# Optimization experiments

Hardware: AMD Instinct MI355X
Metric: run time of the kernel (lower is better)

The kernel has to match this reference:

```python
import jax, jax.numpy as jnp
import numpy as np

N = 20000
E = 320000
IN_DIM = 512
HID = 64
HEADS = 8
OUT_DIM = 40
NEG_SLOPE = 0.2


def glorot(key, shape):
    fan = shape[0] + shape[-1] if len(shape) > 1 else shape[-1]
    s = jnp.sqrt(6.0 / fan)
    return jax.random.uniform(key, shape, jnp.float32, -s, s)


def setup_inputs() -> dict:
    key = jax.random.key(0)
    ks = jax.random.split(key, 12)
    x = jax.random.normal(ks[0], (N, IN_DIM), jnp.float32)
    edge_index = jax.random.randint(ks[1], (2, E), 0, N, jnp.int64)
    return {
        "x": x,
        "edge_index": edge_index,
        "W1": glorot(ks[2], (IN_DIM, HEADS * HID)),
        "att1_src": glorot(ks[3], (HEADS, HID)),
        "att1_dst": glorot(ks[4], (HEADS, HID)),
        "b1": jnp.zeros((HEADS * HID,), jnp.float32),
        "W2": glorot(ks[5], (HEADS * HID, HEADS * HID)),
        "att2_src": glorot(ks[6], (HEADS, HID)),
        "att2_dst": glorot(ks[7], (HEADS, HID)),
        "b2": jnp.zeros((HEADS * HID,), jnp.float32),
        "W3": glorot(ks[8], (HEADS * HID, OUT_DIM)),
        "att3_src": glorot(ks[9], (1, OUT_DIM)),
        "att3_dst": glorot(ks[10], (1, OUT_DIM)),
        "b3": jnp.zeros((OUT_DIM,), jnp.float32),
    }


def gat_conv(x, src, dst, W, att_src, att_dst, bias, heads, out_c):
    # h: [N, H, C] transformed node features
    h = (x @ W).reshape(N, heads, out_c)
    a_src = jnp.sum(h * att_src, axis=-1)  # [N, H]
    a_dst = jnp.sum(h * att_dst, axis=-1)  # [N, H]
    # edge logits (message j=src -> i=dst), softmax grouped by dst
    logits = jax.nn.leaky_relu(a_src[src] + a_dst[dst], NEG_SLOPE)  # [Etot, H]
    seg_max = jax.ops.segment_max(logits, dst, num_segments=N)
    seg_max = jnp.where(jnp.isfinite(seg_max), seg_max, 0.0)
    ex = jnp.exp(logits - seg_max[dst])
    denom = jax.ops.segment_sum(ex, dst, num_segments=N)
    alpha = ex / (denom[dst] + 1e-16)  # [Etot, H]
    msg = h[src] * alpha[:, :, None]  # [Etot, H, C]
    out = jax.ops.segment_sum(msg, dst, num_segments=N)  # [N, H, C]
    return out.reshape(N, heads * out_c) + bias


def reference(x, edge_index, W1, att1_src, att1_dst, b1,
              W2, att2_src, att2_dst, b2,
              W3, att3_src, att3_dst, b3):
    # add self loops (PyG GATConv default)
    loops = jnp.arange(N, dtype=edge_index.dtype)
    src = jnp.concatenate([edge_index[0], loops])
    dst = jnp.concatenate([edge_index[1], loops])
    # dropout layers are identity in eval mode
    h = jax.nn.elu(gat_conv(x, src, dst, W1, att1_src, att1_dst, b1, HEADS, HID))
    h = jax.nn.elu(gat_conv(h, src, dst, W2, att2_src, att2_dst, b2, HEADS, HID))
    h = gat_conv(h, src, dst, W3, att3_src, att3_dst, b3, 1, OUT_DIM)
    return jax.nn.log_softmax(h, axis=-1)
```

## Files before the change

kernel.cpp:

```cpp
#include <hip/hip_runtime.h>
#include <math.h>

#define NN 20000
#define EE 320000
#define ETOT (EE + NN)
#define NEG 0.2f

typedef unsigned short ushortT;
typedef __attribute__((ext_vector_type(8))) short short8v;
typedef __attribute__((ext_vector_type(8))) unsigned short u16x8;
typedef __attribute__((ext_vector_type(4))) float f32x4;

__device__ __forceinline__ ushortT f2b(float f){
  unsigned u = __float_as_uint(f);
  u += 0x7FFFu + ((u >> 16) & 1u);
  return (ushortT)(u >> 16);
}
__device__ __forceinline__ float b2f(ushortT b){
  return __uint_as_float(((unsigned)b) << 16);
}

__global__ void k_cvt(const float* __restrict__ in, ushortT* __restrict__ outp, int n4){
  int i = blockIdx.x*blockDim.x + threadIdx.x;
  if(i < n4){
    float4 v = *reinterpret_cast<const float4*>(in + (size_t)i*4);
    ushort4 o;
    o.x = f2b(v.x); o.y = f2b(v.y); o.z = f2b(v.z); o.w = f2b(v.w);
    *reinterpret_cast<ushort4*>(outp + (size_t)i*4) = o;
  }
}

__global__ void k_wtrans(const float* __restrict__ W, ushortT* __restrict__ Wt){
  __shared__ float t[32][33];
  int bk = blockIdx.x*32, bn = blockIdx.y*32;
  int tx = threadIdx.x & 31, ty = threadIdx.x >> 5;
  for(int r=0;r<32;r+=8)
    t[ty+r][tx] = W[(size_t)(bk+ty+r)*512 + bn+tx];
  __syncthreads();
  for(int r=0;r<32;r+=8)
    Wt[(size_t)(bn+ty+r)*512 + bk+tx] = f2b(t[tx][ty+r]);
}

__global__ void k_wtrans3(const float* __restrict__ W3, ushortT* __restrict__ Wt3p){
  int idx = blockIdx.x*blockDim.x + threadIdx.x;
  if(idx >= 64*48*8) return;
  int kslot = idx / 384;
  int rem = idx - kslot*384;
  int n = rem >> 3;
  int jj = rem & 7;
  int k = kslot*8 + jj;
  float v = (n < 40) ? W3[(size_t)k*40 + n] : 0.f;
  Wt3p[idx] = f2b(v);
}

__global__ void k_count(const int* __restrict__ edst, int* __restrict__ counts){
  int e = blockIdx.x*blockDim.x + threadIdx.x;
  if(e < ETOT){
    int d = (e < EE) ? edst[e] : (e - EE);
    atomicAdd(&counts[d], 1);
  }
}

__global__ void k_scan(const int* __restrict__ counts, int* __restrict__ rowstart){
  __shared__ int lds[1024];
  int tid = threadIdx.x;
  int base = tid*20;
  int s = 0;
  for(int j=0;j<20;j++){ int i=base+j; if(i<NN) s += counts[i]; }
  lds[tid] = s; __syncthreads();
  for(int off=1; off<1024; off<<=1){
    int v = (tid>=off) ? lds[tid-off] : 0;
    __syncthreads();
    lds[tid] += v;
    __syncthreads();
  }
  int run = lds[tid] - s;
  for(int j=0;j<20;j++){
    int i = base+j;
    if(i <= NN){
      rowstart[i] = run;
      if(i < NN) run += counts[i];
    }
  }
}

__global__ void k_fill(const int* __restrict__ esrc, const int* __restrict__ edst,
                       const int* __restrict__ rowstart,
                       int* __restrict__ cursor, int* __restrict__ srcs){
  int e = blockIdx.x*blockDim.x + threadIdx.x;
  if(e < ETOT){
    int d = (e < EE) ? edst[e] : (e - EE);
    int s = (e < EE) ? esrc[e] : (e - EE);
    int pos = rowstart[d] + atomicAdd(&cursor[d], 1);
    srcs[pos] = s;
  }
}

__global__ __launch_bounds__(256) void k_gemm_bf16(
    const ushortT* __restrict__ A, const ushortT* __restrict__ Bt,
    ushortT* __restrict__ Cb, int M)
{
  const int K = 512;
  __shared__ __align__(16) ushortT As[128*32];
  __shared__ __align__(16) ushortT Bs[128*32];
  int bm = blockIdx.x*128, bn = blockIdx.y*128;
  int tid = threadIdx.x, wave = tid>>6, lane = tid&63;
  int wm = (wave>>1)*64, wn = (wave&1)*64;
  f32x4 acc[4][4] = {};

  int l4 = lane>>2;
  int s4 = lane&3;
  int src_slot = s4 ^ (l4 & 3);
  int r16 = lane&15, kg = lane>>4;

  for(int k0=0;k0<K;k0+=32){
    #pragma unroll
    for(int c=0;c<2;c++){
      int chunk = wave*2 + c;
      int arow = bm + chunk*16 + l4; if(arow > M-1) arow = M-1;
      const ushortT* ga = A + (size_t)arow*K + k0 + src_slot*8;
      __builtin_amdgcn_global_load_lds(
          (const __attribute__((address_space(1))) void*)ga,
          (__attribute__((address_space(3))) void*)(As + chunk*16*32), 16, 0, 0);
      int brow = bn + chunk*16 + l4;
      const ushortT* gb = Bt + (size_t)brow*K + k0 + src_slot*8;
      __builtin_amdgcn_global_load_lds(
          (const __attribute__((address_space(1))) void*)gb,
          (__attribute__((address_space(3))) void*)(Bs + chunk*16*32), 16, 0, 0);
    }
    asm volatile("s_waitcnt vmcnt(0)");
    __syncthreads();

    short8v a_frag[4], b_frag[4];
    #pragma unroll
    for(int i=0;i<4;i++){
      int row = wm + i*16 + r16;
      a_frag[i] = *reinterpret_cast<const short8v*>(As + row*32 + ((kg ^ (row&3))<<3));
    }
    #pragma unroll
    for(int j=0;j<4;j++){
      int row = wn + j*16 + r16;
      b_frag[j] = *reinterpret_cast<const short8v*>(Bs + row*32 + ((kg ^ (row&3))<<3));
    }
    #pragma unroll
    for(int i=0;i<4;i++)
      #pragma unroll
      for(int j=0;j<4;j++)
        acc[i][j] = __builtin_amdgcn_mfma_f32_16x16x32_bf16(a_frag[i], b_frag[j], acc[i][j], 0, 0, 0);
    __syncthreads();
  }

  #pragma unroll
  for(int i=0;i<4;i++){
    #pragma unroll
    for(int j=0;j<4;j++){
      #pragma unroll
      for(int r=0;r<4;r++){
        int row = bm + wm + i*16 + kg*4 + r;
        int col = bn + wn + j*16 + r16;
        if(row < M) Cb[(size_t)row*512 + col] = f2b(acc[i][j][r]);
      }
    }
  }
}

__global__ __launch_bounds__(256) void k_gemm3m(const ushortT* __restrict__ A,
                                                const ushortT* __restrict__ Wt3p,
                                                ushortT* __restrict__ Cb, int M){
  const int K = 512;
  __shared__ __align__(16) ushortT As[128*32];
  __shared__ __align__(16) ushortT Bs[64*48*8];
  int bm = blockIdx.x*128;
  int tid = threadIdx.x, wave = tid>>6, lane = tid&63;

  #pragma unroll
  for(int it=0; it<12; it++){
    int o = (it*256 + tid)*8;
    *reinterpret_cast<u16x8*>(Bs + o) = *reinterpret_cast<const u16x8*>(Wt3p + o);
  }

  int l4 = lane>>2, s4 = lane&3;
  int src_slot = s4 ^ (l4 & 3);
  int r16 = lane&15, kg = lane>>4;
  f32x4 acc[2][3] = {};

  for(int k0=0;k0<K;k0+=32){
    #pragma unroll
    for(int c=0;c<2;c++){
      int chunk = wave*2 + c;
      int arow = bm + chunk*16 + l4; if(arow > M-1) arow = M-1;
      const ushortT* ga = A + (size_t)arow*K + k0 + src_slot*8;
      __builtin_amdgcn_global_load_lds(
          (const __attribute__((address_space(1))) void*)ga,
          (__attribute__((address_space(3))) void*)(As + chunk*16*32), 16, 0, 0);
    }
    asm volatile("s_waitcnt vmcnt(0)");
    __syncthreads();

    short8v a_frag[2], b_frag[3];
    #pragma unroll
    for(int i=0;i<2;i++){
      int row = wave*32 + i*16 + r16;
      a_frag[i] = *reinterpret_cast<const short8v*>(As + row*32 + ((kg ^ (row&3))<<3));
    }
    int kslot = (k0>>3) + kg;
    #pragma unroll
    for(int j=0;j<3;j++){
      b_frag[j] = *reinterpret_cast<const short8v*>(Bs + kslot*384 + (j*16 + r16)*8);
    }
    #pragma unroll
    for(int i=0;i<2;i++)
      #pragma unroll
      for(int j=0;j<3;j++)
        acc[i][j] = __builtin_amdgcn_mfma_f32_16x16x32_bf16(a_frag[i], b_frag[j], acc[i][j], 0, 0, 0);
    __syncthreads();
  }

  #pragma unroll
  for(int i=0;i<2;i++){
    #pragma unroll
    for(int j=0;j<3;j++){
      #pragma unroll
      for(int r=0;r<4;r++){
        int row = bm + wave*32 + i*16 + kg*4 + r;
        int col = j*16 + r16;
        if(row < M && col < 40) Cb[(size_t)row*40 + col] = f2b(acc[i][j][r]);
      }
    }
  }
}

__global__ void k_attn8(const ushortT* __restrict__ feat, const float* __restrict__ atts,
                        const float* __restrict__ attd, float* __restrict__ a_s,
                        float* __restrict__ a_d){
  int n = blockIdx.x*4 + (threadIdx.x>>6);
  int lane = threadIdx.x & 63;
  if(n >= NN) return;
  int c0 = lane*8;
  u16x8 v = *reinterpret_cast<const u16x8*>(feat + (size_t)n*512 + c0);
  float s1 = 0.f, s2 = 0.f;
  #pragma unroll
  for(int j=0;j<8;j++){
    float f = b2f((ushortT)v[j]);
    s1 += f*atts[c0+j];
    s2 += f*attd[c0+j];
  }
  #pragma unroll
  for(int off=1; off<8; off<<=1){
    s1 += __shfl_xor(s1, off);
    s2 += __shfl_xor(s2, off);
  }
  if((lane&7) == 0){
    int head = lane>>3;
    a_s[n*8+head] = s1;
    a_d[n*8+head] = s2;
  }
}

__global__ void k_attn1b(const ushortT* __restrict__ feat, const float* __restrict__ atts,
                         const float* __restrict__ attd, float* __restrict__ a_s,
                         float* __restrict__ a_d){
  int n = blockIdx.x*4 + (threadIdx.x>>6);
  int lane = threadIdx.x & 63;
  if(n >= NN) return;
  float s1 = 0.f, s2 = 0.f;
  if(lane < 40){
    float v = b2f(feat[(size_t)n*40 + lane]);
    s1 = v*atts[lane];
    s2 = v*attd[lane];
  }
  for(int off=32; off; off>>=1){
    s1 += __shfl_xor(s1, off);
    s2 += __shfl_xor(s2, off);
  }
  if(lane == 0){ a_s[n] = s1; a_d[n] = s2; }
}

__global__ __launch_bounds__(512) void k_agg512(const ushortT* __restrict__ feat,
    const float* __restrict__ a_s, const float* __restrict__ a_d,
    const int* __restrict__ rowstart, const int* __restrict__ srcs,
    const float* __restrict__ bias, ushortT* __restrict__ outb){
  int slice = blockIdx.x & 7;
  int lane  = threadIdx.x & 63;
  int ds = lane>>3, cg = lane&7;
  int d = (blockIdx.x>>3)*64 + (int)(threadIdx.x>>6)*8 + ds;
  bool dok = d < NN;
  int p  = dok ? rowstart[d]   : 0;
  int p1 = dok ? rowstart[d+1] : 0;
  unsigned cbase = ((unsigned)slice<<6) + ((unsigned)cg<<3);
  float ad_h = dok ? a_d[((unsigned)d<<3) + slice] : 0.f;
  float acc[8] = {0.f,0.f,0.f,0.f,0.f,0.f,0.f,0.f};
  float dsum = 0.f;

  for(; p+4 <= p1; p += 4){
    int s0 = srcs[p],   s1 = srcs[p+1];
    int s2 = srcs[p+2], s3 = srcs[p+3];
    float e0 = a_s[((unsigned)s0<<3) + slice];
    float e1 = a_s[((unsigned)s1<<3) + slice];
    float e2 = a_s[((unsigned)s2<<3) + slice];
    float e3 = a_s[((unsigned)s3<<3) + slice];
    u16x8 v0 = *reinterpret_cast<const u16x8*>(feat + (((unsigned)s0<<9) + cbase));
    u16x8 v1 = *reinterpret_cast<const u16x8*>(feat + (((unsigned)s1<<9) + cbase));
    u16x8 v2 = *reinterpret_cast<const u16x8*>(feat + (((unsigned)s2<<9) + cbase));
    u16x8 v3 = *reinterpret_cast<const u16x8*>(feat + (((unsigned)s3<<9) + cbase));
    float l0 = e0 + ad_h, l1 = e1 + ad_h, l2 = e2 + ad_h, l3 = e3 + ad_h;
    float al0 = __expf(fmaxf(l0, NEG*l0));
    float al1 = __expf(fmaxf(l1, NEG*l1));
    float al2 = __expf(fmaxf(l2, NEG*l2));
    float al3 = __expf(fmaxf(l3, NEG*l3));
    dsum += al0 + al1 + al2 + al3;
    #pragma unroll
    for(int j=0;j<8;j++) acc[j] += al0*b2f((ushortT)v0[j]);
    #pragma unroll
    for(int j=0;j<8;j++) acc[j] += al1*b2f((ushortT)v1[j]);
    #pragma unroll
    for(int j=0;j<8;j++) acc[j] += al2*b2f((ushortT)v2[j]);
    #pragma unroll
    for(int j=0;j<8;j++) acc[j] += al3*b2f((ushortT)v3[j]);
  }
  while(__any(p < p1)){
    bool valid = p < p1;
    int pc = valid ? p : 0;
    int s_ = srcs[pc];
    float e_ = a_s[((unsigned)s_<<3) + slice];
    u16x8 v = *reinterpret_cast<const u16x8*>(feat + (((unsigned)s_<<9) + cbase));
    float l = e_ + ad_h;
    float al = valid ? __expf(fmaxf(l, NEG*l)) : 0.f;
    dsum += al;
    #pragma unroll
    for(int j=0;j<8;j++) acc[j] += al*b2f((ushortT)v[j]);
    p++;
  }

  if(dok){
    float invd = 1.f/(dsum + 1e-16f);
    u16x8 ov;
    #pragma unroll
    for(int j=0;j<8;j++){
      float o = acc[j]*invd + bias[cbase+j];
      o = (o > 0.f) ? o : (__expf(o) - 1.f);
      ov[j] = f2b(o);
    }
    *reinterpret_cast<u16x8*>(outb + (size_t)d*512 + cbase) = ov;
  }
}

__global__ void k_agg_l3(const ushortT* __restrict__ feat,
    const float* __restrict__ a_s, const float* __restrict__ a_d,
    const int* __restrict__ rowstart, const int* __restrict__ srcs,
    const float* __restrict__ bias, float* __restrict__ outp){
  int d = blockIdx.x;
  int lane = threadIdx.x;
  bool act = lane < 40;
  int li = act ? lane : 0;
  float ad_v = a_d[d];
  float acc = 0.f, dsum = 0.f;
  int p0 = rowstart[d], p1 = rowstart[d+1];
  int p = p0;
  for(; p+4 <= p1; p += 4){
    int s0_ = srcs[p], s1_ = srcs[p+1], s2_ = srcs[p+2], s3_ = srcs[p+3];
    float l0 = a_s[s0_] + ad_v, l1 = a_s[s1_] + ad_v;
    float l2 = a_s[s2_] + ad_v, l3 = a_s[s3_] + ad_v;
    float v0 = b2f(feat[(size_t)s0_*40 + li]);
    float v1 = b2f(feat[(size_t)s1_*40 + li]);
    float v2 = b2f(feat[(size_t)s2_*40 + li]);
    float v3 = b2f(feat[(size_t)s3_*40 + li]);
    float al0 = __expf(fmaxf(l0, NEG*l0));
    float al1 = __expf(fmaxf(l1, NEG*l1));
    float al2 = __expf(fmaxf(l2, NEG*l2));
    float al3 = __expf(fmaxf(l3, NEG*l3));
    dsum += al0 + al1 + al2 + al3;
    acc += al0*v0 + al1*v1 + al2*v2 + al3*v3;
  }
  for(; p<p1; p++){
    int s_ = srcs[p];
    float l = a_s[s_] + ad_v;
    float al = __expf(fmaxf(l, NEG*l));
    dsum += al;
    acc += al*b2f(feat[(size_t)s_*40 + li]);
  }
  float invd = 1.f/(dsum + 1e-16f);
  float o = act ? (acc*invd + bias[lane]) : -1e30f;
  float m = o;
  for(int off=32; off; off>>=1) m = fmaxf(m, __shfl_xor(m, off));
  float e_ = act ? expf(o - m) : 0.f;
  float ssum = e_;
  for(int off=32; off; off>>=1) ssum += __shfl_xor(ssum, off);
  if(act) outp[(size_t)d*40 + lane] = o - m - logf(ssum);
}

extern "C" void kernel_launch(void* const* d_in, const int* in_sizes, int n_in,
                              void* d_out, int out_size, void* d_ws, size_t ws_size,
                              hipStream_t stream){
  const float* x   = (const float*)d_in[0];
  const int*   ei  = (const int*)d_in[1];
  const int*   esrc = ei;
  const int*   edst = ei + EE;
  const float* W1  = (const float*)d_in[2];
  const float* as1 = (const float*)d_in[3];
  const float* ad1 = (const float*)d_in[4];
  const float* b1  = (const float*)d_in[5];
  const float* W2  = (const float*)d_in[6];
  const float* as2 = (const float*)d_in[7];
  const float* ad2 = (const float*)d_in[8];
  const float* b2  = (const float*)d_in[9];
  const float* W3  = (const float*)d_in[10];
  const float* as3 = (const float*)d_in[11];
  const float* ad3 = (const float*)d_in[12];
  const float* b3  = (const float*)d_in[13];
  float* out = (float*)d_out;

  char* w = (char*)d_ws;
  size_t off = 0;
  auto alloc = [&](size_t bytes)->char*{
    char* p = w + off;
    off = (off + bytes + 255) & ~(size_t)255;
    return p;
  };
  ushortT*  xb   = (ushortT*)alloc((size_t)NN*512*2);
  ushortT*  fA   = (ushortT*)alloc((size_t)NN*512*2);
  ushortT*  fB   = (ushortT*)alloc((size_t)NN*512*2);
  ushortT*  h3b  = (ushortT*)alloc((size_t)NN*40*2);
  ushortT*  Wt1  = (ushortT*)alloc((size_t)512*512*2);
  ushortT*  Wt2  = (ushortT*)alloc((size_t)512*512*2);
  ushortT*  Wt3p = (ushortT*)alloc((size_t)64*48*8*2);
  float*    a_s  = (float*)alloc((size_t)NN*8*4);
  float*    a_d  = (float*)alloc((size_t)NN*8*4);
  int* rowstart  = (int*)alloc((size_t)(NN+1)*4);
  int* cursor    = (int*)alloc((size_t)NN*4);
  int* counts    = (int*)alloc((size_t)NN*4);
  int* srcs      = (int*)alloc((size_t)ETOT*4);

  k_cvt<<<(NN*512/4 + 255)/256, 256, 0, stream>>>(x, xb, NN*512/4);
  dim3 wt_grid(16, 16);
  k_wtrans<<<wt_grid, 256, 0, stream>>>(W1, Wt1);
  k_wtrans<<<wt_grid, 256, 0, stream>>>(W2, Wt2);
  k_wtrans3<<<(64*48*8 + 255)/256, 256, 0, stream>>>(W3, Wt3p);

  hipMemsetAsync(counts, 0, (size_t)NN*4, stream);
  hipMemsetAsync(cursor, 0, (size_t)NN*4, stream);
  k_count<<<(ETOT+255)/256, 256, 0, stream>>>(edst, counts);
  k_scan<<<1, 1024, 0, stream>>>(counts, rowstart);
  k_fill<<<(ETOT+255)/256, 256, 0, stream>>>(esrc, edst, rowstart, cursor, srcs);

  dim3 mgrid((NN+127)/128, 4);
  int agg_blocks = ((NN + 63)/64)*8;

  k_gemm_bf16<<<mgrid, 256, 0, stream>>>(xb, Wt1, fA, NN);
  k_attn8<<<(NN+3)/4, 256, 0, stream>>>(fA, as1, ad1, a_s, a_d);
  k_agg512<<<agg_blocks, 512, 0, stream>>>(fA, a_s, a_d, rowstart, srcs, b1, fB);

  k_gemm_bf16<<<mgrid, 256, 0, stream>>>(fB, Wt2, fA, NN);
  k_attn8<<<(NN+3)/4, 256, 0, stream>>>(fA, as2, ad2, a_s, a_d);
  k_agg512<<<agg_blocks, 512, 0, stream>>>(fA, a_s, a_d, rowstart, srcs, b2, fB);

  k_gemm3m<<<(NN+127)/128, 256, 0, stream>>>(fB, Wt3p, h3b, NN);
  k_attn1b<<<(NN+3)/4, 256, 0, stream>>>(h3b, as3, ad3, a_s, a_d);
  k_agg_l3<<<NN, 64, 0, stream>>>(h3b, a_s, a_d, rowstart, srcs, b3, out);
}
```

Baseline: 257.9 us.

## Precompute per-edge attention weights and sort destinations by degree for aggregation

Adds a per-edge kernel that computes the exponentiated leaky-relu attention weight for all 8 heads once, stored head-planar, so the aggregation kernel reads contiguous weights instead of gathering a_s per source and running exp redundantly in every lane. It also buckets destination nodes by in-degree and processes them in that order, so the 8 destinations sharing a wave have similar edge counts and less divergence. The cost is an extra ~11 MB weight array written and read per layer, an extra edsts array, and several small preprocessing kernels.

```diff
diff --git a/kernel.cpp b/kernel.cpp
--- a/kernel.cpp
+++ b/kernel.cpp
@@ -86,13 +86,42 @@
 
 __global__ void k_fill(const int* __restrict__ esrc, const int* __restrict__ edst,
                        const int* __restrict__ rowstart,
-                       int* __restrict__ cursor, int* __restrict__ srcs){
+                       int* __restrict__ cursor, int* __restrict__ srcs,
+                       int* __restrict__ edsts){
   int e = blockIdx.x*blockDim.x + threadIdx.x;
   if(e < ETOT){
     int d = (e < EE) ? edst[e] : (e - EE);
     int s = (e < EE) ? esrc[e] : (e - EE);
     int pos = rowstart[d] + atomicAdd(&cursor[d], 1);
     srcs[pos] = s;
+    edsts[pos] = d;
+  }
+}
+
+__global__ void k_dhist(const int* __restrict__ counts, int* __restrict__ dhist){
+  int d = blockIdx.x*blockDim.x + threadIdx.x;
+  if(d < NN){
+    int b = counts[d]; if(b > 63) b = 63;
+    atomicAdd(&dhist[b], 1);
+  }
+}
+__global__ void k_dscan(const int* __restrict__ dhist, int* __restrict__ dbase){
+  int t = threadIdx.x;
+  int v = dhist[t];
+  int sum = v;
+  for(int off=1; off<64; off<<=1){
+    int u = __shfl_up(sum, off);
+    if(t >= off) sum += u;
+  }
+  dbase[t] = sum - v;
+}
+__global__ void k_dscatter(const int* __restrict__ counts, const int* __restrict__ dbase,
+                           int* __restrict__ dcur, int* __restrict__ dorder){
+  int d = blockIdx.x*blockDim.x + threadIdx.x;
+  if(d < NN){
+    int b = counts[d]; if(b > 63) b = 63;
+    int pos = dbase[b] + atomicAdd(&dcur[b], 1);
+    dorder[pos] = d;
   }
 }
 
@@ -276,38 +305,51 @@
   if(lane == 0){ a_s[n] = s1; a_d[n] = s2; }
 }
 
+__global__ void k_edge_pre(const int* __restrict__ srcs, const int* __restrict__ edsts,
+                           const float* __restrict__ a_s, const float* __restrict__ a_d,
+                           float* __restrict__ ap){
+  int pos = blockIdx.x*blockDim.x + threadIdx.x;
+  if(pos >= ETOT) return;
+  int s = srcs[pos], d = edsts[pos];
+  float4 s0 = *reinterpret_cast<const float4*>(a_s + ((size_t)s<<3));
+  float4 s1 = *reinterpret_cast<const float4*>(a_s + ((size_t)s<<3) + 4);
+  float4 d0 = *reinterpret_cast<const float4*>(a_d + ((size_t)d<<3));
+  float4 d1 = *reinterpret_cast<const float4*>(a_d + ((size_t)d<<3) + 4);
+  float l[8] = { s0.x+d0.x, s0.y+d0.y, s0.z+d0.z, s0.w+d0.w,
+                 s1.x+d1.x, s1.y+d1.y, s1.z+d1.z, s1.w+d1.w };
+  #pragma unroll
+  for(int h=0;h<8;h++){
+    float al = __expf(fmaxf(l[h], NEG*l[h]));
+    ap[(size_t)h*ETOT + pos] = al;
+  }
+}
+
 __global__ __launch_bounds__(512) void k_agg512(const ushortT* __restrict__ feat,
-    const float* __restrict__ a_s, const float* __restrict__ a_d,
-    const int* __restrict__ rowstart, const int* __restrict__ srcs,
+    const float* __restrict__ ap, const int* __restrict__ rowstart,
+    const int* __restrict__ srcs, const int* __restrict__ dorder,
     const float* __restrict__ bias, ushortT* __restrict__ outb){
   int slice = blockIdx.x & 7;
   int lane  = threadIdx.x & 63;
   int ds = lane>>3, cg = lane&7;
-  int d = (blockIdx.x>>3)*64 + (int)(threadIdx.x>>6)*8 + ds;
-  bool dok = d < NN;
+  int idx = (blockIdx.x>>3)*64 + (int)(threadIdx.x>>6)*8 + ds;
+  bool dok = idx < NN;
+  int d  = dok ? dorder[idx] : 0;
   int p  = dok ? rowstart[d]   : 0;
   int p1 = dok ? rowstart[d+1] : 0;
+  const float* plane = ap + (size_t)slice*ETOT;
   unsigned cbase = ((unsigned)slice<<6) + ((unsigned)cg<<3);
-  float ad_h = dok ? a_d[((unsigned)d<<3) + slice] : 0.f;
   float acc[8] = {0.f,0.f,0.f,0.f,0.f,0.f,0.f,0.f};
   float dsum = 0.f;
 
   for(; p+4 <= p1; p += 4){
     int s0 = srcs[p],   s1 = srcs[p+1];
     int s2 = srcs[p+2], s3 = srcs[p+3];
-    float e0 = a_s[((unsigned)s0<<3) + slice];
-    float e1 = a_s[((unsigned)s1<<3) + slice];
-    float e2 = a_s[((unsigned)s2<<3) + slice];
-    float e3 = a_s[((unsigned)s3<<3) + slice];
+    float al0 = plane[p],   al1 = plane[p+1];
+    float al2 = plane[p+2], al3 = plane[p+3];
     u16x8 v0 = *reinterpret_cast<const u16x8*>(feat + (((unsigned)s0<<9) + cbase));
     u16x8 v1 = *reinterpret_cast<const u16x8*>(feat + (((unsigned)s1<<9) + cbase));
     u16x8 v2 = *reinterpret_cast<const u16x8*>(feat + (((unsigned)s2<<9) + cbase));
     u16x8 v3 = *reinterpret_cast<const u16x8*>(feat + (((unsigned)s3<<9) + cbase));
-    float l0 = e0 + ad_h, l1 = e1 + ad_h, l2 = e2 + ad_h, l3 = e3 + ad_h;
-    float al0 = __expf(fmaxf(l0, NEG*l0));
-    float al1 = __expf(fmaxf(l1, NEG*l1));
-    float al2 = __expf(fmaxf(l2, NEG*l2));
-    float al3 = __expf(fmaxf(l3, NEG*l3));
     dsum += al0 + al1 + al2 + al3;
     #pragma unroll
     for(int j=0;j<8;j++) acc[j] += al0*b2f((ushortT)v0[j]);
@@ -322,10 +364,8 @@
     bool valid = p < p1;
     int pc = valid ? p : 0;
     int s_ = srcs[pc];
-    float e_ = a_s[((unsigned)s_<<3) + slice];
+    float al = valid ? plane[pc] : 0.f;
     u16x8 v = *reinterpret_cast<const u16x8*>(feat + (((unsigned)s_<<9) + cbase));
-    float l = e_ + ad_h;
-    float al = valid ? __expf(fmaxf(l, NEG*l)) : 0.f;
     dsum += al;
     #pragma unroll
     for(int j=0;j<8;j++) acc[j] += al*b2f((ushortT)v[j]);
@@ -426,10 +466,16 @@
   ushortT*  Wt3p = (ushortT*)alloc((size_t)64*48*8*2);
   float*    a_s  = (float*)alloc((size_t)NN*8*4);
   float*    a_d  = (float*)alloc((size_t)NN*8*4);
+  float*    ap   = (float*)alloc((size_t)8*ETOT*4);
   int* rowstart  = (int*)alloc((size_t)(NN+1)*4);
   int* cursor    = (int*)alloc((size_t)NN*4);
   int* counts    = (int*)alloc((size_t)NN*4);
   int* srcs      = (int*)alloc((size_t)ETOT*4);
+  int* edsts     = (int*)alloc((size_t)ETOT*4);
+  int* dorder    = (int*)alloc((size_t)NN*4);
+  int* dhist     = (int*)alloc((size_t)64*4);
+  int* dbase     = (int*)alloc((size_t)64*4);
+  int* dcur      = (int*)alloc((size_t)64*4);
 
   k_cvt<<<(NN*512/4 + 255)/256, 256, 0, stream>>>(x, xb, NN*512/4);
   dim3 wt_grid(16, 16);
@@ -439,20 +485,29 @@
 
   hipMemsetAsync(counts, 0, (size_t)NN*4, stream);
   hipMemsetAsync(cursor, 0, (size_t)NN*4, stream);
+  hipMemsetAsync(dhist,  0, (size_t)64*4, stream);
+  hipMemsetAsync(dcur,   0, (size_t)64*4, stream);
   k_count<<<(ETOT+255)/256, 256, 0, stream>>>(edst, counts);
   k_scan<<<1, 1024, 0, stream>>>(counts, rowstart);
-  k_fill<<<(ETOT+255)/256, 256, 0, stream>>>(esrc, edst, rowstart, cursor, srcs);
+  k_fill<<<(ETOT+255)/256, 256, 0, stream>>>(esrc, edst, rowstart, cursor, srcs, edsts);
+
+  k_dhist<<<(NN+255)/256, 256, 0, stream>>>(counts, dhist);
+  k_dscan<<<1, 64, 0, stream>>>(dhist, dbase);
+  k_dscatter<<<(NN+255)/256, 256, 0, stream>>>(counts, dbase, dcur, dorder);
 
   dim3 mgrid((NN+127)/128, 4);
-  int agg_blocks = ((NN + 63)/64)*8;
+  int edge_blocks = (ETOT + 255)/256;
+  int agg_blocks  = ((NN + 63)/64)*8;
 
   k_gemm_bf16<<<mgrid, 256, 0, stream>>>(xb, Wt1, fA, NN);
   k_attn8<<<(NN+3)/4, 256, 0, stream>>>(fA, as1, ad1, a_s, a_d);
-  k_agg512<<<agg_blocks, 512, 0, stream>>>(fA, a_s, a_d, rowstart, srcs, b1, fB);
+  k_edge_pre<<<edge_blocks, 256, 0, stream>>>(srcs, edsts, a_s, a_d, ap);
+  k_agg512<<<agg_blocks, 512, 0, stream>>>(fA, ap, rowstart, srcs, dorder, b1, fB);
 
   k_gemm_bf16<<<mgrid, 256, 0, stream>>>(fB, Wt2, fA, NN);
   k_attn8<<<(NN+3)/4, 256, 0, stream>>>(fA, as2, ad2, a_s, a_d);
-  k_agg512<<<agg_blocks, 512, 0, stream>>>(fA, a_s, a_d, rowstart, srcs, b2, fB);
+  k_edge_pre<<<edge_blocks, 256, 0, stream>>>(srcs, edsts, a_s, a_d, ap);
+  k_agg512<<<agg_blocks, 512, 0, stream>>>(fA, ap, rowstart, srcs, dorder, b2, fB);
 
   k_gemm3m<<<(NN+127)/128, 256, 0, stream>>>(fB, Wt3p, h3b, NN);
   k_attn1b<<<(NN+3)/4, 256, 0, stream>>>(h3b, as3, ad3, a_s, a_d);
```

New measurement: 374.6 us. 1.45x slower.

## Precompute per-edge attention weights packed with source index before aggregation

Applied to the files above, without the earlier changes.

Adds an edge pre-pass that computes the unnormalized exp(leaky_relu) attention per head for each CSR edge. It packs that weight as bf16 together with the 16-bit source index into a head-major record array, which k_agg512 then reads with a single load per edge instead of a srcs load, a dependent a_s gather and an exp. The aim is to shorten the dependent-load chain and cut redundant exp work in the aggregation kernels. The cost is an extra kernel per layer and an 8×ETOT uint buffer written and read back. Attention weights also drop to bf16 precision, and the packing relies on node indices fitting in 16 bits (N=20000 fits).

```diff
diff --git a/kernel.cpp b/kernel.cpp
--- a/kernel.cpp
+++ b/kernel.cpp
@@ -86,13 +86,15 @@
 
 __global__ void k_fill(const int* __restrict__ esrc, const int* __restrict__ edst,
                        const int* __restrict__ rowstart,
-                       int* __restrict__ cursor, int* __restrict__ srcs){
+                       int* __restrict__ cursor, int* __restrict__ srcs,
+                       int* __restrict__ edsts){
   int e = blockIdx.x*blockDim.x + threadIdx.x;
   if(e < ETOT){
     int d = (e < EE) ? edst[e] : (e - EE);
     int s = (e < EE) ? esrc[e] : (e - EE);
     int pos = rowstart[d] + atomicAdd(&cursor[d], 1);
     srcs[pos] = s;
+    edsts[pos] = d;
   }
 }
 
@@ -276,9 +278,28 @@
   if(lane == 0){ a_s[n] = s1; a_d[n] = s2; }
 }
 
+__global__ void k_edge_pre(const int* __restrict__ srcs, const int* __restrict__ edsts,
+                           const float* __restrict__ a_s, const float* __restrict__ a_d,
+                           unsigned* __restrict__ rec){
+  int pos = blockIdx.x*blockDim.x + threadIdx.x;
+  if(pos >= ETOT) return;
+  int s = srcs[pos], d = edsts[pos];
+  float4 s0 = *reinterpret_cast<const float4*>(a_s + ((size_t)s<<3));
+  float4 s1 = *reinterpret_cast<const float4*>(a_s + ((size_t)s<<3) + 4);
+  float4 d0 = *reinterpret_cast<const float4*>(a_d + ((size_t)d<<3));
+  float4 d1 = *reinterpret_cast<const float4*>(a_d + ((size_t)d<<3) + 4);
+  float l[8] = { s0.x+d0.x, s0.y+d0.y, s0.z+d0.z, s0.w+d0.w,
+                 s1.x+d1.x, s1.y+d1.y, s1.z+d1.z, s1.w+d1.w };
+  unsigned sh = ((unsigned)s) << 16;
+  #pragma unroll
+  for(int h=0;h<8;h++){
+    float al = __expf(fmaxf(l[h], NEG*l[h]));
+    rec[(size_t)h*ETOT + pos] = sh | (unsigned)f2b(al);
+  }
+}
+
 __global__ __launch_bounds__(512) void k_agg512(const ushortT* __restrict__ feat,
-    const float* __restrict__ a_s, const float* __restrict__ a_d,
-    const int* __restrict__ rowstart, const int* __restrict__ srcs,
+    const unsigned* __restrict__ rec, const int* __restrict__ rowstart,
     const float* __restrict__ bias, ushortT* __restrict__ outb){
   int slice = blockIdx.x & 7;
   int lane  = threadIdx.x & 63;
@@ -287,27 +308,24 @@
   bool dok = d < NN;
   int p  = dok ? rowstart[d]   : 0;
   int p1 = dok ? rowstart[d+1] : 0;
+  const unsigned* plane = rec + (size_t)slice*ETOT;
   unsigned cbase = ((unsigned)slice<<6) + ((unsigned)cg<<3);
-  float ad_h = dok ? a_d[((unsigned)d<<3) + slice] : 0.f;
   float acc[8] = {0.f,0.f,0.f,0.f,0.f,0.f,0.f,0.f};
   float dsum = 0.f;
 
   for(; p+4 <= p1; p += 4){
-    int s0 = srcs[p],   s1 = srcs[p+1];
-    int s2 = srcs[p+2], s3 = srcs[p+3];
-    float e0 = a_s[((unsigned)s0<<3) + slice];
-    float e1 = a_s[((unsigned)s1<<3) + slice];
-    float e2 = a_s[((unsigned)s2<<3) + slice];
-    float e3 = a_s[((unsigned)s3<<3) + slice];
-    u16x8 v0 = *reinterpret_cast<const u16x8*>(feat + (((unsigned)s0<<9) + cbase));
-    u16x8 v1 = *reinterpret_cast<const u16x8*>(feat + (((unsigned)s1<<9) + cbase));
-    u16x8 v2 = *reinterpret_cast<const u16x8*>(feat + (((unsigned)s2<<9) + cbase));
-    u16x8 v3 = *reinterpret_cast<const u16x8*>(feat + (((unsigned)s3<<9) + cbase));
-    float l0 = e0 + ad_h, l1 = e1 + ad_h, l2 = e2 + ad_h, l3 = e3 + ad_h;
-    float al0 = __expf(fmaxf(l0, NEG*l0));
-    float al1 = __expf(fmaxf(l1, NEG*l1));
-    float al2 = __expf(fmaxf(l2, NEG*l2));
-    float al3 = __expf(fmaxf(l3, NEG*l3));
+    unsigned r0 = plane[p];
+    unsigned r1 = plane[p+1];
+    unsigned r2 = plane[p+2];
+    unsigned r3 = plane[p+3];
+    u16x8 v0 = *reinterpret_cast<const u16x8*>(feat + ((r0>>16<<9) + cbase));
+    u16x8 v1 = *reinterpret_cast<const u16x8*>(feat + ((r1>>16<<9) + cbase));
+    u16x8 v2 = *reinterpret_cast<const u16x8*>(feat + ((r2>>16<<9) + cbase));
+    u16x8 v3 = *reinterpret_cast<const u16x8*>(feat + ((r3>>16<<9) + cbase));
+    float al0 = b2f((ushortT)(r0 & 0xffffu));
+    float al1 = b2f((ushortT)(r1 & 0xffffu));
+    float al2 = b2f((ushortT)(r2 & 0xffffu));
+    float al3 = b2f((ushortT)(r3 & 0xffffu));
     dsum += al0 + al1 + al2 + al3;
     #pragma unroll
     for(int j=0;j<8;j++) acc[j] += al0*b2f((ushortT)v0[j]);
@@ -321,11 +339,9 @@
   while(__any(p < p1)){
     bool valid = p < p1;
     int pc = valid ? p : 0;
-    int s_ = srcs[pc];
-    float e_ = a_s[((unsigned)s_<<3) + slice];
-    u16x8 v = *reinterpret_cast<const u16x8*>(feat + (((unsigned)s_<<9) + cbase));
-    float l = e_ + ad_h;
-    float al = valid ? __expf(fmaxf(l, NEG*l)) : 0.f;
+    unsigned r = plane[pc];
+    float al = valid ? b2f((ushortT)(r & 0xffffu)) : 0.f;
+    u16x8 v = *reinterpret_cast<const u16x8*>(feat + ((r>>16<<9) + cbase));
     dsum += al;
     #pragma unroll
     for(int j=0;j<8;j++) acc[j] += al*b2f((ushortT)v[j]);
@@ -426,10 +442,12 @@
   ushortT*  Wt3p = (ushortT*)alloc((size_t)64*48*8*2);
   float*    a_s  = (float*)alloc((size_t)NN*8*4);
   float*    a_d  = (float*)alloc((size_t)NN*8*4);
+  unsigned* rec  = (unsigned*)alloc((size_t)8*ETOT*4);
   int* rowstart  = (int*)alloc((size_t)(NN+1)*4);
   int* cursor    = (int*)alloc((size_t)NN*4);
   int* counts    = (int*)alloc((size_t)NN*4);
   int* srcs      = (int*)alloc((size_t)ETOT*4);
+  int* edsts     = (int*)alloc((size_t)ETOT*4);
 
   k_cvt<<<(NN*512/4 + 255)/256, 256, 0, stream>>>(x, xb, NN*512/4);
   dim3 wt_grid(16, 16);
@@ -441,18 +459,21 @@
   hipMemsetAsync(cursor, 0, (size_t)NN*4, stream);
   k_count<<<(ETOT+255)/256, 256, 0, stream>>>(edst, counts);
   k_scan<<<1, 1024, 0, stream>>>(counts, rowstart);
-  k_fill<<<(ETOT+255)/256, 256, 0, stream>>>(esrc, edst, rowstart, cursor, srcs);
+  k_fill<<<(ETOT+255)/256, 256, 0, stream>>>(esrc, edst, rowstart, cursor, srcs, edsts);
 
   dim3 mgrid((NN+127)/128, 4);
-  int agg_blocks = ((NN + 63)/64)*8;
+  int edge_blocks = (ETOT + 255)/256;
+  int agg_blocks  = ((NN + 63)/64)*8;
 
   k_gemm_bf16<<<mgrid, 256, 0, stream>>>(xb, Wt1, fA, NN);
   k_attn8<<<(NN+3)/4, 256, 0, stream>>>(fA, as1, ad1, a_s, a_d);
-  k_agg512<<<agg_blocks, 512, 0, stream>>>(fA, a_s, a_d, rowstart, srcs, b1, fB);
+  k_edge_pre<<<edge_blocks, 256, 0, stream>>>(srcs, edsts, a_s, a_d, rec);
+  k_agg512<<<agg_blocks, 512, 0, stream>>>(fA, rec, rowstart, b1, fB);
 
   k_gemm_bf16<<<mgrid, 256, 0, stream>>>(fB, Wt2, fA, NN);
   k_attn8<<<(NN+3)/4, 256, 0, stream>>>(fA, as2, ad2, a_s, a_d);
-  k_agg512<<<agg_blocks, 512, 0, stream>>>(fA, a_s, a_d, rowstart, srcs, b2, fB);
+  k_edge_pre<<<edge_blocks, 256, 0, stream>>>(srcs, edsts, a_s, a_d, rec);
+  k_agg512<<<agg_blocks, 512, 0, stream>>>(fA, rec, rowstart, b2, fB);
 
   k_gemm3m<<<(NN+127)/128, 256, 0, stream>>>(fB, Wt3p, h3b, NN);
   k_attn1b<<<(NN+3)/4, 256, 0, stream>>>(h3b, as3, ad3, a_s, a_d);
```

Measured after the change: 240.1 us. -6.9%, faster.
